# Performance work log

Hardware: AMD Instinct MI355X
Metric: run time of the kernel (lower is better)

Reference implementation:

```python
import jax, jax.numpy as jnp
import numpy as np

T, HID, H, HKV, D = 4096, 2048, 16, 2, 128
EPS = 1e-6


def setup_inputs() -> dict:
    key = jax.random.key(0)
    ks = jax.random.split(key, 5)
    hidden_states = jax.random.normal(ks[0], (T, HID), dtype=jnp.float32)
    # rope angles: build realistic cos/sin from positions and inv-freqs
    inv_freq = 1.0 / (10000.0 ** (jnp.arange(0, D, 2, dtype=jnp.float32) / D))
    ang = jnp.arange(T, dtype=jnp.float32)[:, None] * inv_freq[None, :]  # [T, D/2]
    ang = jnp.concatenate([ang, ang], axis=-1)  # [T, D]
    cos, sin = jnp.cos(ang), jnp.sin(ang)
    w_qkv = jax.random.normal(ks[1], (HID, (2 * H + 2 * HKV) * D), dtype=jnp.float32) * (HID ** -0.5)
    w_o = jax.random.normal(ks[2], (H * D, HID), dtype=jnp.float32) * ((H * D) ** -0.5)
    q_norm_w = jnp.ones((D,), dtype=jnp.float32)
    k_norm_w = jnp.ones((D,), dtype=jnp.float32)
    return {"hidden_states": hidden_states, "cos": cos, "sin": sin,
            "w_qkv": w_qkv, "w_o": w_o, "q_norm_w": q_norm_w, "k_norm_w": k_norm_w}


def _rms_norm(x, w):
    var = jnp.mean(x * x, axis=-1, keepdims=True)
    return x * jax.lax.rsqrt(var + EPS) * w


def _rotate_half(x):
    x1, x2 = x[..., : D // 2], x[..., D // 2:]
    return jnp.concatenate([-x2, x1], axis=-1)


def _rope(x, cos, sin):
    # x: [T, h, D]; cos/sin: [T, D]
    return x * cos[:, None, :] + _rotate_half(x) * sin[:, None, :]


def reference(hidden_states, cos, sin, w_qkv, w_o, q_norm_w, k_norm_w):
    qkv = hidden_states @ w_qkv  # [T, (2H+2HKV)*D]
    q_sz, kv_sz = 2 * H * D, HKV * D
    # packed query+gate: view as [T, H, 2D], first half query, second half gate
    qg = qkv[:, :q_sz].reshape(T, H, 2 * D)
    q, gate = qg[..., :D], qg[..., D:]
    k = qkv[:, q_sz:q_sz + kv_sz].reshape(T, HKV, D)
    v = qkv[:, q_sz + kv_sz:].reshape(T, HKV, D)
    q = _rms_norm(q, q_norm_w)
    k = _rms_norm(k, k_norm_w)
    q = _rope(q, cos, sin)
    k = _rope(k, cos, sin)
    # GQA: expand kv heads to H
    rep = H // HKV
    k = jnp.repeat(k, rep, axis=1)  # [T, H, D]
    v = jnp.repeat(v, rep, axis=1)
    scale = D ** -0.5
    scores = jnp.einsum('thd,shd->hts', q, k) * scale  # [H, T, T]
    causal = jnp.tril(jnp.ones((T, T), dtype=bool))
    scores = jnp.where(causal[None], scores, jnp.finfo(scores.dtype).min)
    probs = jax.nn.softmax(scores, axis=-1)
    attn = jnp.einsum('hts,shd->thd', probs, v)  # [T, H, D]
    out = attn.reshape(T, H * D) * jax.nn.sigmoid(gate.reshape(T, H * D))
    return out @ w_o
```

## Files before the change

### kernel.cpp

```cpp
#include <hip/hip_runtime.h>
#include <hip/hip_bf16.h>
#include <math.h>


namespace {
constexpr int kT   = 4096;
constexpr int kHid = 2048;
constexpr int kH   = 16;
constexpr int kHkv = 2;
constexpr int kD   = 128;
constexpr int kNqkv = (2 * kH + 2 * kHkv) * kD;
constexpr int kQsz  = 2 * kH * kD;
constexpr int kRowU = kNqkv * 2;
constexpr float kEps = 1e-6f;
constexpr float kScale = 0.08838834764831845f;
}

typedef __attribute__((ext_vector_type(8))) short short8;
typedef __attribute__((ext_vector_type(4))) float floatx4;

__device__ inline unsigned short f2bf(float x) {
  unsigned u = __float_as_uint(x);
  u = (u + 0x7fffu + ((u >> 16) & 1u)) >> 16;
  return (unsigned short)u;
}

__device__ inline void gload_lds16(const void* g, void* l) {
  typedef const __attribute__((address_space(1))) unsigned GQ;
  typedef __attribute__((address_space(3))) unsigned LQ;
  __builtin_amdgcn_global_load_lds((GQ*)g, (LQ*)l, 16, 0, 0);
}

__global__ __launch_bounds__(256)
void cvt_bf16(const float* __restrict__ in, unsigned short* __restrict__ out,
              long nelem) {
  long i = ((long)blockIdx.x * 256 + threadIdx.x) * 4;
  if (i >= nelem) return;
  float4 v = *(const float4*)(in + i);
  unsigned long long p = (unsigned long long)f2bf(v.x) |
                         ((unsigned long long)f2bf(v.y) << 16) |
                         ((unsigned long long)f2bf(v.z) << 32) |
                         ((unsigned long long)f2bf(v.w) << 48);
  *(unsigned long long*)(out + i) = p;
}

__global__ __launch_bounds__(256)
void transpose_cvt(const float* __restrict__ in, unsigned short* __restrict__ out,
                   int R, int C) {
  __shared__ float t[32][33];
  const int bx = blockIdx.x * 32;
  const int by = blockIdx.y * 32;
  const int x = threadIdx.x & 31, y = threadIdx.x >> 5;
#pragma unroll
  for (int j = 0; j < 4; ++j)
    t[y * 4 + j][x] = in[(long)(by + y * 4 + j) * C + bx + x];
  __syncthreads();
#pragma unroll
  for (int j = 0; j < 4; ++j)
    out[(long)(bx + y * 4 + j) * R + by + x] = f2bf(t[x][y * 4 + j]);
}

__global__ __launch_bounds__(256)
void vt_transpose(const float* __restrict__ qkv, unsigned short* __restrict__ VtG) {
  __shared__ float t[32][33];
  const int t0 = blockIdx.x * 32;
  const int c0 = blockIdx.y * 32;
  const int x = threadIdx.x & 31, y = threadIdx.x >> 5;
#pragma unroll
  for (int j = 0; j < 4; ++j)
    t[y * 4 + j][x] = qkv[(long)(t0 + y * 4 + j) * kNqkv + 4352 + c0 + x];
  __syncthreads();
#pragma unroll
  for (int j = 0; j < 4; ++j)
    VtG[(long)(c0 + y * 4 + j) * kT + t0 + x] = f2bf(t[x][y * 4 + j]);
}

__global__ __launch_bounds__(256)
void gemm_bf16(const unsigned short* __restrict__ A,
               const unsigned short* __restrict__ Bt, float* __restrict__ C,
               int M, int N, int K) {
  __shared__ __align__(16) unsigned short As[128 * 64];
  __shared__ __align__(16) unsigned short Bs[128 * 64];
  const int tid = threadIdx.x;
  const int lane = tid & 63;
  const int w = tid >> 6;
  const int wr = w >> 1, wc = w & 1;
  const int n = lane & 15;
  const int quad = lane >> 4;
  const long bm = (long)blockIdx.x * 128, bn = (long)blockIdx.y * 128;

  floatx4 acc[4][4];
  floatx4 zero = {0.f, 0.f, 0.f, 0.f};
#pragma unroll
  for (int a = 0; a < 4; ++a)
#pragma unroll
    for (int b = 0; b < 4; ++b) acc[a][b] = zero;

  for (int k0 = 0; k0 < K; k0 += 64) {
    __syncthreads();
#pragma unroll
    for (int it = 0; it < 4; ++it) {
      int ci = it * 256 + tid;
      int r = ci >> 3, c = ci & 7;
      int cg = c ^ (r & 7);
      gload_lds16(A + (bm + r) * (long)K + k0 + cg * 8, As + (it * 256 + w * 64) * 8);
      gload_lds16(Bt + (bn + r) * (long)K + k0 + cg * 8, Bs + (it * 256 + w * 64) * 8);
    }
    __syncthreads();

#pragma unroll
    for (int ks = 0; ks < 2; ++ks) {
      short8 af[4], bf[4];
#pragma unroll
      for (int a = 0; a < 4; ++a) {
        int m = wr * 64 + a * 16 + n;
        af[a] = *(const short8*)(As + m * 64 + ((4 * ks + quad) ^ (m & 7)) * 8);
      }
#pragma unroll
      for (int b = 0; b < 4; ++b) {
        int nn = wc * 64 + b * 16 + n;
        bf[b] = *(const short8*)(Bs + nn * 64 + ((4 * ks + quad) ^ (nn & 7)) * 8);
      }
#pragma unroll
      for (int a = 0; a < 4; ++a)
#pragma unroll
        for (int b = 0; b < 4; ++b)
          acc[a][b] = __builtin_amdgcn_mfma_f32_16x16x32_bf16(af[a], bf[b], acc[a][b], 0, 0, 0);
    }
  }
#pragma unroll
  for (int a = 0; a < 4; ++a)
#pragma unroll
    for (int b = 0; b < 4; ++b)
#pragma unroll
      for (int r = 0; r < 4; ++r)
        C[(bm + wr * 64 + a * 16 + quad * 4 + r) * (long)N + bn + wc * 64 + b * 16 + n] =
            acc[a][b][r];
}

__global__ __launch_bounds__(128)
void norm_rope_cvt(float* qkv, const float* __restrict__ cosb,
                   const float* __restrict__ sinb, const float* __restrict__ qw,
                   const float* __restrict__ kw) {
  unsigned short* qkvu = (unsigned short*)qkv;
  const int blk = blockIdx.x;
  const int t = blk / 18;
  const int h = blk % 18;
  const int i = threadIdx.x;

  const bool isq = (h < kH);
  const long base = (long)t * kNqkv + (isq ? h * 2 * kD : kQsz + (h - kH) * kD);
  float x = qkv[base + i];
  float v = x * x;
#pragma unroll
  for (int off = 1; off < 64; off <<= 1) v += __shfl_xor(v, off, 64);
  __shared__ float wsum[2];
  if ((i & 63) == 0) wsum[i >> 6] = v;
  __syncthreads();
  float rms = rsqrtf((wsum[0] + wsum[1]) * (1.0f / kD) + kEps);
  float nv = x * rms * (isq ? qw[i] : kw[i]);
  __shared__ float nb[128];
  nb[i] = nv;
  __syncthreads();
  float rot = (i < 64) ? -nb[i + 64] : nb[i - 64];
  float ro = nv * cosb[t * kD + i] + rot * sinb[t * kD + i];
  if (isq) {
    float g = qkv[base + kD + i];
    qkv[base + kD + i] = 1.0f / (1.0f + __expf(-g));
    qkvu[(long)t * kRowU + 512 * h + i] = f2bf(ro);
  } else {
    qkvu[(long)t * kRowU + 8192 + 256 * (h - kH) + i] = f2bf(ro);
  }
}

__global__ __launch_bounds__(256)
void flash_attn_mfma(const unsigned short* qkvu, const float* qkvf,
                     const unsigned short* VtG, unsigned short* __restrict__ og) {
  __shared__ __align__(16) unsigned short Ks[64 * 128];
  __shared__ __align__(16) unsigned short Vt[128 * 64];

  const int tid = threadIdx.x;
  const int lane = tid & 63;
  const int w = tid >> 6;
  const int n = lane & 15;
  const int quad = lane >> 4;
  const int g = blockIdx.x;
  const int h = g & 15;
  const int bm = 31 - (g >> 4);
  const int hk = h >> 3;
  const int q0 = bm * 128;

  short8 qf[2][4];
#pragma unroll
  for (int mt = 0; mt < 2; ++mt) {
    const unsigned short* qrow =
        qkvu + (long)(q0 + 32 * w + 16 * mt + n) * kRowU + 512 * h;
#pragma unroll
    for (int ks = 0; ks < 4; ++ks)
      qf[mt][ks] = *(const short8*)(qrow + 32 * ks + 8 * quad);
  }
  short8 lfrag;
  {
    short o = (n == 0) ? (short)0x3F80 : (short)0;
    lfrag = (short8){o, o, o, o, o, o, o, o};
  }

  floatx4 O[2][8];
  floatx4 Ol[2];
  floatx4 zero = {0.f, 0.f, 0.f, 0.f};
#pragma unroll
  for (int mt = 0; mt < 2; ++mt) {
    Ol[mt] = zero;
#pragma unroll
    for (int dt = 0; dt < 8; ++dt) O[mt][dt] = zero;
  }

  const int kn_end = 2 * bm + 1;
  for (int kn = 0; kn <= kn_end; ++kn) {
    __syncthreads();
#pragma unroll
    for (int it = 0; it < 4; ++it) {
      int pc = (w * 4 + it) * 64 + lane;
      int r = pc >> 4, c = pc & 15;
      int lc = c ^ (r & 15);
      gload_lds16(qkvu + (long)(kn * 64 + r) * kRowU + 8192 + 256 * hk + 8 * lc,
                  Ks + (w * 4 + it) * 512);
    }
#pragma unroll
    for (int it = 0; it < 4; ++it) {
      int pc = (w * 4 + it) * 64 + lane;
      int d = pc >> 3, c = pc & 7;
      int lc = c ^ (d & 7);
      gload_lds16(VtG + (long)hk * (128 * kT) + (long)d * kT + kn * 64 + 8 * lc,
                  Vt + (w * 4 + it) * 512);
    }
    __syncthreads();

    floatx4 S[2][4];
#pragma unroll
    for (int mt = 0; mt < 2; ++mt)
#pragma unroll
      for (int ct = 0; ct < 4; ++ct) S[mt][ct] = zero;
#pragma unroll
    for (int ks = 0; ks < 4; ++ks) {
#pragma unroll
      for (int ct = 0; ct < 4; ++ct) {
        int row = 16 * ct + n;
        short8 kf = *(const short8*)(Ks + row * 128 + ((4 * ks + quad) ^ n) * 8);
        S[0][ct] = __builtin_amdgcn_mfma_f32_16x16x32_bf16(qf[0][ks], kf, S[0][ct], 0, 0, 0);
        S[1][ct] = __builtin_amdgcn_mfma_f32_16x16x32_bf16(qf[1][ks], kf, S[1][ct], 0, 0, 0);
      }
    }
    __syncthreads();

    unsigned short* Ps = Ks;
    const bool needmask = (kn >= 2 * bm);
    const int jbase = (kn - 2 * bm) * 64;
    const int hi = n >> 3, lo = n & 7;
#pragma unroll
    for (int mt = 0; mt < 2; ++mt) {
#pragma unroll
      for (int r = 0; r < 4; ++r) {
        int prow = 32 * w + 16 * mt + quad * 4 + r;
        float p0 = __expf(S[mt][0][r] * kScale);
        float p1 = __expf(S[mt][1][r] * kScale);
        float p2 = __expf(S[mt][2][r] * kScale);
        float p3 = __expf(S[mt][3][r] * kScale);
        if (needmask) {
          if (jbase + n > prow) p0 = 0.f;
          if (jbase + 16 + n > prow) p1 = 0.f;
          if (jbase + 32 + n > prow) p2 = 0.f;
          if (jbase + 48 + n > prow) p3 = 0.f;
        }
        int sw = prow & 7;
        Ps[prow * 64 + (((0 + hi) ^ sw) << 3) + lo] = f2bf(p0);
        Ps[prow * 64 + (((2 + hi) ^ sw) << 3) + lo] = f2bf(p1);
        Ps[prow * 64 + (((4 + hi) ^ sw) << 3) + lo] = f2bf(p2);
        Ps[prow * 64 + (((6 + hi) ^ sw) << 3) + lo] = f2bf(p3);
      }
    }
    __asm__ volatile("s_waitcnt lgkmcnt(0)" ::: "memory");

#pragma unroll
    for (int ks = 0; ks < 2; ++ks) {
      int r0 = 32 * w + n, r1 = 32 * w + 16 + n;
      short8 pf0 = *(const short8*)(Ps + r0 * 64 + (((4 * ks + quad) ^ (r0 & 7)) << 3));
      short8 pf1 = *(const short8*)(Ps + r1 * 64 + (((4 * ks + quad) ^ (r1 & 7)) << 3));
      Ol[0] = __builtin_amdgcn_mfma_f32_16x16x32_bf16(pf0, lfrag, Ol[0], 0, 0, 0);
      Ol[1] = __builtin_amdgcn_mfma_f32_16x16x32_bf16(pf1, lfrag, Ol[1], 0, 0, 0);
#pragma unroll
      for (int dt = 0; dt < 8; ++dt) {
        int d = 16 * dt + n;
        short8 vf = *(const short8*)(Vt + d * 64 + (((4 * ks + quad) ^ (d & 7)) << 3));
        O[0][dt] = __builtin_amdgcn_mfma_f32_16x16x32_bf16(pf0, vf, O[0][dt], 0, 0, 0);
        O[1][dt] = __builtin_amdgcn_mfma_f32_16x16x32_bf16(pf1, vf, O[1][dt], 0, 0, 0);
      }
    }
  }

#pragma unroll
  for (int mt = 0; mt < 2; ++mt) {
#pragma unroll
    for (int r = 0; r < 4; ++r) {
      float l = __shfl(Ol[mt][r], quad << 4, 64);
      float inv = 1.0f / l;
      int row = q0 + 32 * w + 16 * mt + quad * 4 + r;
#pragma unroll
      for (int dt = 0; dt < 8; ++dt) {
        int col = 16 * dt + n;
        float gte = qkvf[(long)row * kNqkv + 256 * h + 128 + col];
        og[(long)row * kHid + 128 * h + col] = f2bf(O[mt][dt][r] * inv * gte);
      }
    }
  }
}

extern "C" void kernel_launch(void* const* d_in, const int* in_sizes, int n_in,
                              void* d_out, int out_size, void* d_ws, size_t ws_size,
                              hipStream_t stream) {
  (void)in_sizes; (void)n_in; (void)out_size; (void)ws_size;
  const float* hs   = (const float*)d_in[0];
  const float* cosb = (const float*)d_in[1];
  const float* sinb = (const float*)d_in[2];
  const float* wqkv = (const float*)d_in[3];
  const float* wo   = (const float*)d_in[4];
  const float* qw   = (const float*)d_in[5];
  const float* kw   = (const float*)d_in[6];
  float* out = (float*)d_out;

  char* ws = (char*)d_ws;
  float* qkv = (float*)ws;
  unsigned short* hsb = (unsigned short*)(ws + 75497472);
  unsigned short* og  = hsb;
  unsigned short* wt  = (unsigned short*)(ws + 92274688);
  unsigned short* VtG = wt;

  cvt_bf16<<<dim3(8192), 256, 0, stream>>>(hs, hsb, (long)kT * kHid);
  transpose_cvt<<<dim3(kNqkv / 32, kHid / 32), 256, 0, stream>>>(wqkv, wt, kHid, kNqkv);
  gemm_bf16<<<dim3(kT / 128, kNqkv / 128), 256, 0, stream>>>(hsb, wt, qkv, kT, kNqkv, kHid);
  vt_transpose<<<dim3(kT / 32, 8), 256, 0, stream>>>(qkv, VtG);
  norm_rope_cvt<<<dim3(kT * 18), 128, 0, stream>>>(qkv, cosb, sinb, qw, kw);
  flash_attn_mfma<<<dim3(kT / 128 * kH), 256, 0, stream>>>((const unsigned short*)qkv, qkv, VtG, og);
  transpose_cvt<<<dim3(kHid / 32, kHid / 32), 256, 0, stream>>>(wo, wt, kHid, kHid);
  gemm_bf16<<<dim3(kT / 128, kHid / 128), 256, 0, stream>>>(og, wt, out, kT, kHid, kHid);
}
```

Measured before the change: 503.7 us.

## Double-buffer K/V tiles in flash attention and balance causal block order

```diff
diff --git a/kernel.cpp b/kernel.cpp
--- a/kernel.cpp
+++ b/kernel.cpp
@@ -176,8 +176,8 @@
 __global__ __launch_bounds__(256)
 void flash_attn_mfma(const unsigned short* qkvu, const float* qkvf,
                      const unsigned short* VtG, unsigned short* __restrict__ og) {
-  __shared__ __align__(16) unsigned short Ks[64 * 128];
-  __shared__ __align__(16) unsigned short Vt[128 * 64];
+  __shared__ __align__(16) unsigned short Ks[2][64 * 128];
+  __shared__ __align__(16) unsigned short Vt[2][128 * 64];
 
   const int tid = threadIdx.x;
   const int lane = tid & 63;
@@ -186,7 +186,8 @@
   const int quad = lane >> 4;
   const int g = blockIdx.x;
   const int h = g & 15;
-  const int bm = 31 - (g >> 4);
+  const int gi = g >> 4;
+  const int bm = (gi < 16) ? (31 - gi) : (gi - 16);
   const int hk = h >> 3;
   const int q0 = bm * 128;
 
@@ -215,16 +216,14 @@
     for (int dt = 0; dt < 8; ++dt) O[mt][dt] = zero;
   }
 
-  const int kn_end = 2 * bm + 1;
-  for (int kn = 0; kn <= kn_end; ++kn) {
-    __syncthreads();
+  auto stage = [&](int b, int kn) {
 #pragma unroll
     for (int it = 0; it < 4; ++it) {
       int pc = (w * 4 + it) * 64 + lane;
       int r = pc >> 4, c = pc & 15;
       int lc = c ^ (r & 15);
       gload_lds16(qkvu + (long)(kn * 64 + r) * kRowU + 8192 + 256 * hk + 8 * lc,
-                  Ks + (w * 4 + it) * 512);
+                  &Ks[b][(w * 4 + it) * 512]);
     }
 #pragma unroll
     for (int it = 0; it < 4; ++it) {
@@ -232,28 +231,49 @@
       int d = pc >> 3, c = pc & 7;
       int lc = c ^ (d & 7);
       gload_lds16(VtG + (long)hk * (128 * kT) + (long)d * kT + kn * 64 + 8 * lc,
-                  Vt + (w * 4 + it) * 512);
-    }
-    __syncthreads();
+                  &Vt[b][(w * 4 + it) * 512]);
+    }
+  };
+
+  const int kn_end = 2 * bm + 1;
+  stage(0, 0);
+
+  for (int kn = 0; kn <= kn_end; ++kn) {
+    const int cur = kn & 1;
+    if (kn < kn_end) {
+      stage(cur ^ 1, kn + 1);
+      __asm__ volatile("s_waitcnt vmcnt(8)" ::: "memory");
+    } else {
+      __asm__ volatile("s_waitcnt vmcnt(0)" ::: "memory");
+    }
+    __builtin_amdgcn_s_barrier();
+    __builtin_amdgcn_sched_barrier(0);
+
+    const unsigned short* Kc = Ks[cur];
+    const unsigned short* Vc = Vt[cur];
 
     floatx4 S[2][4];
 #pragma unroll
     for (int mt = 0; mt < 2; ++mt)
 #pragma unroll
       for (int ct = 0; ct < 4; ++ct) S[mt][ct] = zero;
+    __builtin_amdgcn_s_setprio(1);
 #pragma unroll
     for (int ks = 0; ks < 4; ++ks) {
 #pragma unroll
       for (int ct = 0; ct < 4; ++ct) {
         int row = 16 * ct + n;
-        short8 kf = *(const short8*)(Ks + row * 128 + ((4 * ks + quad) ^ n) * 8);
+        short8 kf = *(const short8*)(Kc + row * 128 + ((4 * ks + quad) ^ n) * 8);
         S[0][ct] = __builtin_amdgcn_mfma_f32_16x16x32_bf16(qf[0][ks], kf, S[0][ct], 0, 0, 0);
         S[1][ct] = __builtin_amdgcn_mfma_f32_16x16x32_bf16(qf[1][ks], kf, S[1][ct], 0, 0, 0);
       }
     }
-    __syncthreads();
-
-    unsigned short* Ps = Ks;
+    __builtin_amdgcn_s_setprio(0);
+    __asm__ volatile("s_waitcnt lgkmcnt(0)" ::: "memory");
+    __builtin_amdgcn_s_barrier();
+    __builtin_amdgcn_sched_barrier(0);
+
+    unsigned short* Ps = (unsigned short*)Kc;
     const bool needmask = (kn >= 2 * bm);
     const int jbase = (kn - 2 * bm) * 64;
     const int hi = n >> 3, lo = n & 7;
@@ -280,7 +300,9 @@
       }
     }
     __asm__ volatile("s_waitcnt lgkmcnt(0)" ::: "memory");
-
+    __builtin_amdgcn_sched_barrier(0);
+
+    __builtin_amdgcn_s_setprio(1);
 #pragma unroll
     for (int ks = 0; ks < 2; ++ks) {
       int r0 = 32 * w + n, r1 = 32 * w + 16 + n;
@@ -291,11 +313,15 @@
 #pragma unroll
       for (int dt = 0; dt < 8; ++dt) {
         int d = 16 * dt + n;
-        short8 vf = *(const short8*)(Vt + d * 64 + (((4 * ks + quad) ^ (d & 7)) << 3));
+        short8 vf = *(const short8*)(Vc + d * 64 + (((4 * ks + quad) ^ (d & 7)) << 3));
         O[0][dt] = __builtin_amdgcn_mfma_f32_16x16x32_bf16(pf0, vf, O[0][dt], 0, 0, 0);
         O[1][dt] = __builtin_amdgcn_mfma_f32_16x16x32_bf16(pf1, vf, O[1][dt], 0, 0, 0);
       }
     }
+    __builtin_amdgcn_s_setprio(0);
+    __asm__ volatile("s_waitcnt lgkmcnt(0)" ::: "memory");
+    __builtin_amdgcn_s_barrier();
+    __builtin_amdgcn_sched_barrier(0);
   }
 
 #pragma unroll
```

Result: slower. 554.7 us (+10.1%).

## Load K and V fragments directly from global memory instead of LDS staging

Applied to the files above, without the earlier changes.

```diff
diff --git a/kernel.cpp b/kernel.cpp
--- a/kernel.cpp
+++ b/kernel.cpp
@@ -176,8 +176,7 @@
 __global__ __launch_bounds__(256)
 void flash_attn_mfma(const unsigned short* qkvu, const float* qkvf,
                      const unsigned short* VtG, unsigned short* __restrict__ og) {
-  __shared__ __align__(16) unsigned short Ks[64 * 128];
-  __shared__ __align__(16) unsigned short Vt[128 * 64];
+  __shared__ __align__(16) unsigned short Ps[128 * 64];
 
   const int tid = threadIdx.x;
   const int lane = tid & 63;
@@ -190,6 +189,9 @@
   const int hk = h >> 3;
   const int q0 = bm * 128;
 
+  const unsigned short* Kg = qkvu + 8192 + 256 * hk;
+  const unsigned short* Vg = VtG + (long)hk * (128 * kT);
+
   short8 qf[2][4];
 #pragma unroll
   for (int mt = 0; mt < 2; ++mt) {
@@ -217,25 +219,6 @@
 
   const int kn_end = 2 * bm + 1;
   for (int kn = 0; kn <= kn_end; ++kn) {
-    __syncthreads();
-#pragma unroll
-    for (int it = 0; it < 4; ++it) {
-      int pc = (w * 4 + it) * 64 + lane;
-      int r = pc >> 4, c = pc & 15;
-      int lc = c ^ (r & 15);
-      gload_lds16(qkvu + (long)(kn * 64 + r) * kRowU + 8192 + 256 * hk + 8 * lc,
-                  Ks + (w * 4 + it) * 512);
-    }
-#pragma unroll
-    for (int it = 0; it < 4; ++it) {
-      int pc = (w * 4 + it) * 64 + lane;
-      int d = pc >> 3, c = pc & 7;
-      int lc = c ^ (d & 7);
-      gload_lds16(VtG + (long)hk * (128 * kT) + (long)d * kT + kn * 64 + 8 * lc,
-                  Vt + (w * 4 + it) * 512);
-    }
-    __syncthreads();
-
     floatx4 S[2][4];
 #pragma unroll
     for (int mt = 0; mt < 2; ++mt)
@@ -245,15 +228,13 @@
     for (int ks = 0; ks < 4; ++ks) {
 #pragma unroll
       for (int ct = 0; ct < 4; ++ct) {
-        int row = 16 * ct + n;
-        short8 kf = *(const short8*)(Ks + row * 128 + ((4 * ks + quad) ^ n) * 8);
+        short8 kf = *(const short8*)(
+            Kg + (long)(kn * 64 + 16 * ct + n) * kRowU + (4 * ks + quad) * 8);
         S[0][ct] = __builtin_amdgcn_mfma_f32_16x16x32_bf16(qf[0][ks], kf, S[0][ct], 0, 0, 0);
         S[1][ct] = __builtin_amdgcn_mfma_f32_16x16x32_bf16(qf[1][ks], kf, S[1][ct], 0, 0, 0);
       }
     }
-    __syncthreads();
-
-    unsigned short* Ps = Ks;
+
     const bool needmask = (kn >= 2 * bm);
     const int jbase = (kn - 2 * bm) * 64;
     const int hi = n >> 3, lo = n & 7;
@@ -290,8 +271,8 @@
       Ol[1] = __builtin_amdgcn_mfma_f32_16x16x32_bf16(pf1, lfrag, Ol[1], 0, 0, 0);
 #pragma unroll
       for (int dt = 0; dt < 8; ++dt) {
-        int d = 16 * dt + n;
-        short8 vf = *(const short8*)(Vt + d * 64 + (((4 * ks + quad) ^ (d & 7)) << 3));
+        short8 vf = *(const short8*)(
+            Vg + (long)(16 * dt + n) * kT + kn * 64 + (4 * ks + quad) * 8);
         O[0][dt] = __builtin_amdgcn_mfma_f32_16x16x32_bf16(pf0, vf, O[0][dt], 0, 0, 0);
         O[1][dt] = __builtin_amdgcn_mfma_f32_16x16x32_bf16(pf1, vf, O[1][dt], 0, 0, 0);
       }
```

Result: slower. 766.4 us (+52.2%).

## Use wave-per-row norm/rope with grid-stride loop and separate P buffer in attention

Applied to the files above, without the earlier changes.

```diff
diff --git a/kernel.cpp b/kernel.cpp
--- a/kernel.cpp
+++ b/kernel.cpp
@@ -138,38 +138,43 @@
             acc[a][b][r];
 }
 
-__global__ __launch_bounds__(128)
+__global__ __launch_bounds__(256)
 void norm_rope_cvt(float* qkv, const float* __restrict__ cosb,
                    const float* __restrict__ sinb, const float* __restrict__ qw,
                    const float* __restrict__ kw) {
   unsigned short* qkvu = (unsigned short*)qkv;
-  const int blk = blockIdx.x;
-  const int t = blk / 18;
-  const int h = blk % 18;
-  const int i = threadIdx.x;
-
-  const bool isq = (h < kH);
-  const long base = (long)t * kNqkv + (isq ? h * 2 * kD : kQsz + (h - kH) * kD);
-  float x = qkv[base + i];
-  float v = x * x;
-#pragma unroll
-  for (int off = 1; off < 64; off <<= 1) v += __shfl_xor(v, off, 64);
-  __shared__ float wsum[2];
-  if ((i & 63) == 0) wsum[i >> 6] = v;
-  __syncthreads();
-  float rms = rsqrtf((wsum[0] + wsum[1]) * (1.0f / kD) + kEps);
-  float nv = x * rms * (isq ? qw[i] : kw[i]);
-  __shared__ float nb[128];
-  nb[i] = nv;
-  __syncthreads();
-  float rot = (i < 64) ? -nb[i + 64] : nb[i - 64];
-  float ro = nv * cosb[t * kD + i] + rot * sinb[t * kD + i];
-  if (isq) {
-    float g = qkv[base + kD + i];
-    qkv[base + kD + i] = 1.0f / (1.0f + __expf(-g));
-    qkvu[(long)t * kRowU + 512 * h + i] = f2bf(ro);
-  } else {
-    qkvu[(long)t * kRowU + 8192 + 256 * (h - kH) + i] = f2bf(ro);
+  const int lane = threadIdx.x & 63;
+  const int wslot = blockIdx.x * 4 + (threadIdx.x >> 6);
+  const int nslots = gridDim.x * 4;
+  for (int task = wslot; task < kT * 18; task += nslots) {
+    const int t = task / 18;
+    const int h = task % 18;
+    const bool isq = (h < kH);
+    const long base = (long)t * kNqkv + (isq ? h * 2 * kD : kQsz + (h - kH) * kD);
+    float xlo = qkv[base + lane];
+    float xhi = qkv[base + 64 + lane];
+    float v = xlo * xlo + xhi * xhi;
+#pragma unroll
+    for (int off = 1; off < 64; off <<= 1) v += __shfl_xor(v, off, 64);
+    float rms = rsqrtf(v * (1.0f / kD) + kEps);
+    const float* wv = isq ? qw : kw;
+    float nlo = xlo * rms * wv[lane];
+    float nhi = xhi * rms * wv[64 + lane];
+    float clo = cosb[t * kD + lane], chi = cosb[t * kD + 64 + lane];
+    float slo = sinb[t * kD + lane], shi = sinb[t * kD + 64 + lane];
+    float rlo = nlo * clo - nhi * slo;
+    float rhi = nhi * chi + nlo * shi;
+    if (isq) {
+      float glo = qkv[base + kD + lane];
+      float ghi = qkv[base + kD + 64 + lane];
+      qkv[base + kD + lane] = 1.0f / (1.0f + __expf(-glo));
+      qkv[base + kD + 64 + lane] = 1.0f / (1.0f + __expf(-ghi));
+      qkvu[(long)t * kRowU + 512 * h + lane] = f2bf(rlo);
+      qkvu[(long)t * kRowU + 512 * h + 64 + lane] = f2bf(rhi);
+    } else {
+      qkvu[(long)t * kRowU + 8192 + 256 * (h - kH) + lane] = f2bf(rlo);
+      qkvu[(long)t * kRowU + 8192 + 256 * (h - kH) + 64 + lane] = f2bf(rhi);
+    }
   }
 }
 
@@ -178,6 +183,7 @@
                      const unsigned short* VtG, unsigned short* __restrict__ og) {
   __shared__ __align__(16) unsigned short Ks[64 * 128];
   __shared__ __align__(16) unsigned short Vt[128 * 64];
+  __shared__ __align__(16) unsigned short Ps[128 * 64];
 
   const int tid = threadIdx.x;
   const int lane = tid & 63;
@@ -251,9 +257,7 @@
         S[1][ct] = __builtin_amdgcn_mfma_f32_16x16x32_bf16(qf[1][ks], kf, S[1][ct], 0, 0, 0);
       }
     }
-    __syncthreads();
-
-    unsigned short* Ps = Ks;
+
     const bool needmask = (kn >= 2 * bm);
     const int jbase = (kn - 2 * bm) * 64;
     const int hi = n >> 3, lo = n & 7;
@@ -339,7 +343,7 @@
   transpose_cvt<<<dim3(kNqkv / 32, kHid / 32), 256, 0, stream>>>(wqkv, wt, kHid, kNqkv);
   gemm_bf16<<<dim3(kT / 128, kNqkv / 128), 256, 0, stream>>>(hsb, wt, qkv, kT, kNqkv, kHid);
   vt_transpose<<<dim3(kT / 32, 8), 256, 0, stream>>>(qkv, VtG);
-  norm_rope_cvt<<<dim3(kT * 18), 128, 0, stream>>>(qkv, cosb, sinb, qw, kw);
+  norm_rope_cvt<<<dim3(2304), 256, 0, stream>>>(qkv, cosb, sinb, qw, kw);
   flash_attn_mfma<<<dim3(kT / 128 * kH), 256, 0, stream>>>((const unsigned short*)qkv, qkv, VtG, og);
   transpose_cvt<<<dim3(kHid / 32, kHid / 32), 256, 0, stream>>>(wo, wt, kHid, kHid);
   gemm_bf16<<<dim3(kT / 128, kHid / 128), 256, 0, stream>>>(og, wt, out, kT, kHid, kHid);
```

Measured after the change: 483.3 us. -4.1%, faster.
